# Kernel tuning notes

Measured on AMD Instinct MI355X. Metric: run time of the kernel, lower is better.

## Reference

```python
import jax, jax.numpy as jnp
import numpy as np

G = 1.0  # gravitational constant (matches init kwarg G=1.0)
EPS = 0.0  # no epsilon in original


def setup_inputs() -> dict:
    key = jax.random.key(0)
    k1, k2 = jax.random.split(key)
    B = 2_000_000
    y = jax.random.normal(k1, (B, 12), dtype=jnp.float32)
    # masses in (0.5, 1.5) to keep r**-3 well behaved
    M = jax.random.uniform(k2, (3,), dtype=jnp.float32, minval=0.5, maxval=1.5)
    t = 0
    return {"y": y, "M": M, "t": t}


def reference(y, M, t):
    # y: [B, 12] = (x1, y1, x2, y2, x3, y3, px1, py1, px2, py2, px3, py3)
    # Faithful to: build A(r12, r13, r23), return y @ A.T  -- expressed
    # without materializing the [B,12,12] A, since A has fixed sparsity.
    del t  # unused, as in the original forward
    p1 = y[:, 0:2]
    p2 = y[:, 2:4]
    p3 = y[:, 4:6]
    r12 = jnp.linalg.norm(p1 - p2, axis=-1)  # [B]
    r13 = jnp.linalg.norm(p1 - p3, axis=-1)
    r23 = jnp.linalg.norm(p2 - p3, axis=-1)
    M0, M1, M2 = M[0], M[1], M[2]
    a = G * M0 * M1 / r12 ** 3  # coupling 1-2, [B]
    b = G * M0 * M2 / r13 ** 3  # coupling 1-3
    c = G * M1 * M2 / r23 ** 3  # coupling 2-3
    x1, y1_, x2, y2_, x3, y3_ = (y[:, i] for i in range(6))
    # dq/dt = p / m  (rows 0..5 of A)
    dq = jnp.stack([y[:, 6] / M0, y[:, 7] / M0,
                    y[:, 8] / M1, y[:, 9] / M1,
                    y[:, 10] / M2, y[:, 11] / M2], axis=-1)
    # dp/dt = gravitational forces (rows 6..11 of A)
    dp = jnp.stack([
        -(a + b) * x1 + a * x2 + b * x3,
        -(a + b) * y1_ + a * y2_ + b * y3_,
        a * x1 - (a + c) * x2 + c * x3,
        a * y1_ - (a + c) * y2_ + c * y3_,
        b * x1 + c * x2 - (b + c) * x3,
        b * y1_ + c * y2_ - (b + c) * y3_,
    ], axis=-1)
    return jnp.concatenate([dq, dp], axis=-1)  # [B, 12]
```

## Files before the change

kernel.cpp:

```cpp
#include <hip/hip_runtime.h>

__global__ __launch_bounds__(256) void ham3body_kernel(
    const float* __restrict__ y,
    const float* __restrict__ M,
    float* __restrict__ out,
    int B)
{
    int i = blockIdx.x * blockDim.x + threadIdx.x;
    if (i >= B) return;

    const float4* yv = reinterpret_cast<const float4*>(y + (size_t)i * 12);
    float4 v0 = yv[0];
    float4 v1 = yv[1];
    float4 v2 = yv[2];

    float x1 = v0.x, y1 = v0.y, x2 = v0.z, y2 = v0.w;
    float x3 = v1.x, y3 = v1.y;
    float p1x = v1.z, p1y = v1.w;
    float p2x = v2.x, p2y = v2.y, p3x = v2.z, p3y = v2.w;

    float M0 = M[0], M1 = M[1], M2 = M[2];

    float dx12 = x1 - x2, dy12 = y1 - y2;
    float dx13 = x1 - x3, dy13 = y1 - y3;
    float dx23 = x2 - x3, dy23 = y2 - y3;

    float s12 = dx12 * dx12 + dy12 * dy12;
    float s13 = dx13 * dx13 + dy13 * dy13;
    float s23 = dx23 * dx23 + dy23 * dy23;

    float a = (M0 * M1) / (s12 * sqrtf(s12));
    float b = (M0 * M2) / (s13 * sqrtf(s13));
    float c = (M1 * M2) / (s23 * sqrtf(s23));

    float4 o0, o1, o2;
    o0.x = p1x / M0;
    o0.y = p1y / M0;
    o0.z = p2x / M1;
    o0.w = p2y / M1;
    o1.x = p3x / M2;
    o1.y = p3y / M2;
    o1.z = -(a + b) * x1 + a * x2 + b * x3;
    o1.w = -(a + b) * y1 + a * y2 + b * y3;
    o2.x = a * x1 - (a + c) * x2 + c * x3;
    o2.y = a * y1 - (a + c) * y2 + c * y3;
    o2.z = b * x1 + c * x2 - (b + c) * x3;
    o2.w = b * y1 + c * y2 - (b + c) * y3;

    float4* ov = reinterpret_cast<float4*>(out + (size_t)i * 12);
    ov[0] = o0;
    ov[1] = o1;
    ov[2] = o2;
}

extern "C" void kernel_launch(void* const* d_in, const int* in_sizes, int n_in,
                              void* d_out, int out_size, void* d_ws, size_t ws_size,
                              hipStream_t stream) {
    const float* y = (const float*)d_in[0];
    const float* M = (const float*)d_in[1];
    float* out = (float*)d_out;

    int B = in_sizes[0] / 12;
    int block = 256;
    int grid = (B + block - 1) / block;
    ham3body_kernel<<<grid, block, 0, stream>>>(y, M, out, B);
}
```

Baseline: 36.24 us.

## Stage loads/stores through LDS for coalescing; use rsq and reciprocal masses

Each block now loads its 768 float4s contiguously into shared memory, so every thread reads consecutive float4s instead of a 48-byte stride, and writes results back through LDS the same way. The divisions are replaced by the hardware reciprocal square root cubed and precomputed inverse masses. This adds LDS traffic and three barriers, and the rsq approximation may lose a little accuracy.

```diff
diff --git a/kernel.cpp b/kernel.cpp
--- a/kernel.cpp
+++ b/kernel.cpp
@@ -1,25 +1,36 @@
 #include <hip/hip_runtime.h>
 
 __global__ __launch_bounds__(256) void ham3body_kernel(
-    const float* __restrict__ y,
+    const float4* __restrict__ y4,
     const float* __restrict__ M,
-    float* __restrict__ out,
+    float4* __restrict__ o4,
     int B)
 {
-    int i = blockIdx.x * blockDim.x + threadIdx.x;
-    if (i >= B) return;
+    __shared__ float4 lds[768];
 
-    const float4* yv = reinterpret_cast<const float4*>(y + (size_t)i * 12);
-    float4 v0 = yv[0];
-    float4 v1 = yv[1];
-    float4 v2 = yv[2];
+    const int t = threadIdx.x;
+    const long nf4 = (long)B * 3;
+    const long base = (long)blockIdx.x * 768;
+
+#pragma unroll
+    for (int k = 0; k < 3; ++k) {
+        long idx = base + k * 256 + t;
+        if (idx < nf4) lds[k * 256 + t] = y4[idx];
+    }
+
+    const float M0 = M[0], M1 = M[1], M2 = M[2];
+    const float invM0 = 1.0f / M0, invM1 = 1.0f / M1, invM2 = 1.0f / M2;
+
+    __syncthreads();
+
+    float4 v0 = lds[t * 3 + 0];
+    float4 v1 = lds[t * 3 + 1];
+    float4 v2 = lds[t * 3 + 2];
 
     float x1 = v0.x, y1 = v0.y, x2 = v0.z, y2 = v0.w;
     float x3 = v1.x, y3 = v1.y;
     float p1x = v1.z, p1y = v1.w;
     float p2x = v2.x, p2y = v2.y, p3x = v2.z, p3y = v2.w;
-
-    float M0 = M[0], M1 = M[1], M2 = M[2];
 
     float dx12 = x1 - x2, dy12 = y1 - y2;
     float dx13 = x1 - x3, dy13 = y1 - y3;
@@ -29,17 +40,20 @@
     float s13 = dx13 * dx13 + dy13 * dy13;
     float s23 = dx23 * dx23 + dy23 * dy23;
 
-    float a = (M0 * M1) / (s12 * sqrtf(s12));
-    float b = (M0 * M2) / (s13 * sqrtf(s13));
-    float c = (M1 * M2) / (s23 * sqrtf(s23));
+    float i12 = __builtin_amdgcn_rsqf(s12);
+    float i13 = __builtin_amdgcn_rsqf(s13);
+    float i23 = __builtin_amdgcn_rsqf(s23);
+    float a = (M0 * M1) * (i12 * i12 * i12);
+    float b = (M0 * M2) * (i13 * i13 * i13);
+    float c = (M1 * M2) * (i23 * i23 * i23);
 
     float4 o0, o1, o2;
-    o0.x = p1x / M0;
-    o0.y = p1y / M0;
-    o0.z = p2x / M1;
-    o0.w = p2y / M1;
-    o1.x = p3x / M2;
-    o1.y = p3y / M2;
+    o0.x = p1x * invM0;
+    o0.y = p1y * invM0;
+    o0.z = p2x * invM1;
+    o0.w = p2y * invM1;
+    o1.x = p3x * invM2;
+    o1.y = p3y * invM2;
     o1.z = -(a + b) * x1 + a * x2 + b * x3;
     o1.w = -(a + b) * y1 + a * y2 + b * y3;
     o2.x = a * x1 - (a + c) * x2 + c * x3;
@@ -47,18 +61,27 @@
     o2.z = b * x1 + c * x2 - (b + c) * x3;
     o2.w = b * y1 + c * y2 - (b + c) * y3;
 
-    float4* ov = reinterpret_cast<float4*>(out + (size_t)i * 12);
-    ov[0] = o0;
-    ov[1] = o1;
-    ov[2] = o2;
+    __syncthreads();
+
+    lds[t * 3 + 0] = o0;
+    lds[t * 3 + 1] = o1;
+    lds[t * 3 + 2] = o2;
+
+    __syncthreads();
+
+#pragma unroll
+    for (int k = 0; k < 3; ++k) {
+        long idx = base + k * 256 + t;
+        if (idx < nf4) o4[idx] = lds[k * 256 + t];
+    }
 }
 
 extern "C" void kernel_launch(void* const* d_in, const int* in_sizes, int n_in,
                               void* d_out, int out_size, void* d_ws, size_t ws_size,
                               hipStream_t stream) {
-    const float* y = (const float*)d_in[0];
+    const float4* y = (const float4*)d_in[0];
     const float* M = (const float*)d_in[1];
-    float* out = (float*)d_out;
+    float4* out = (float4*)d_out;
 
     int B = in_sizes[0] / 12;
     int block = 256;
```

After: 33.84 us. 1.07x faster.
